# Kernel tuning notes

Hardware: AMD Instinct MI355X
Metric: run time of the kernel (lower is better)

The kernel has to match this reference:

```python
import jax, jax.numpy as jnp
import numpy as np


def setup_inputs() -> dict:
    key = jax.random.key(0)
    kx, ka, kb, kc = jax.random.split(key, 4)
    B, S = 32, 16384
    K, L, M = 4, 10, 10
    return {
        "x": jax.random.normal(kx, (B, S, 2), dtype=jnp.float32),
        "a": jax.random.normal(ka, (K, L), dtype=jnp.float32),
        "b": jax.random.normal(kb, (K, L, M), dtype=jnp.float32),
        "c": jax.random.normal(kc, (K, L, M), dtype=jnp.float32),  # unused in forward (matches original)
    }


def reference(x, a, b, c):
    # Generalized Memory Polynomial.
    # y[n] = sum_{k,l} a[k,l] * x[n-L+1+l] * |x[n-L+1+l]|^k
    #      + sum_{k,l,m} b[k,l,m] * x[n-l] * |x[n-l-(m+1)]|^(k+1), for n >= L+M, else 0.
    K, L = a.shape
    M = b.shape[2]
    B, S, _ = x.shape
    D = L + M  # max shift needed is (L-1)+M < D

    xc = x[..., 0] + 1j * x[..., 1]  # (B, S) complex64

    # Shifted views: xs[d][:, n] = x[:, n-d] (zero for n < d; masked out below anyway).
    xp = jnp.pad(xc, ((0, 0), (D - 1, 0)))
    xs = jnp.stack([xp[:, D - 1 - d: D - 1 - d + S] for d in range(D)])  # (D, B, S)

    absx = jnp.abs(xs)  # (D, B, S)
    # pows[k, d] = |x[n-d]|^k, k in 0..K
    pows = absx[None] ** jnp.arange(K + 1, dtype=x.dtype)[:, None, None, None]  # (K+1, D, B, S)

    # Term 1: shift d = L-1-l  ->  coefficient a[k, L-1-d]
    a_rev = a[:, ::-1]  # (K, L), a_rev[k, d] = a[k, L-1-d]
    coef1 = jnp.einsum('kd,kdbs->dbs', a_rev, pows[:K, :L])  # real (L, B, S)
    y = jnp.einsum('dbs,dbs->bs', coef1.astype(xc.dtype), xs[:L])  # complex (B, S)

    # Term 2: y += sum_{k,l,m} b[k,l,m] * x[n-l] * |x[n-l-m-1]|^(k+1)
    for l in range(L):  # small structural loop (L=10)
        coef2 = jnp.einsum('km,kmbs->bs', b[:, l, :], pows[1:, l + 1: l + 1 + M])  # real (B, S)
        y = y + coef2.astype(xc.dtype) * xs[l]

    # Only n >= L+M is written in the original (y initialized to zero elsewhere).
    mask = (jnp.arange(S) >= D).astype(x.dtype)  # (S,)
    y = y * mask

    out = jnp.stack([jnp.real(y), jnp.imag(y)], axis=-1)  # (B, S, 2)
    return out
```

## Files before the change

kernel.cpp:

```cpp
#include <hip/hip_runtime.h>


typedef short short8 __attribute__((ext_vector_type(8)));
typedef float f32x4 __attribute__((ext_vector_type(4)));

constexpr int S_FIXED = 16384;
constexpr int BLK = 256;
constexpr int TILE = 512;

__device__ __forceinline__ unsigned short bfc(float f) {
    union { float f; unsigned u; } v; v.f = f;
    const unsigned u = v.u;
    return (unsigned short)((u + 0x7FFFu + ((u >> 16) & 1u)) >> 16);
}

__device__ __forceinline__ short8 mk8(ushort4 lo, ushort4 hi) {
    union { ushort4 u[2]; short8 s; } x;
    x.u[0] = lo; x.u[1] = hi;
    return x.s;
}

__global__ __launch_bounds__(BLK) void gmp_mfma(
    const float* __restrict__ x,
    const float* __restrict__ a,
    const float* __restrict__ b,
    float* __restrict__ out,
    int S)
{
    __shared__ alignas(16) unsigned short th[16][64];
    __shared__ alignas(16) ushort4 qr[4][160];
    __shared__ alignas(16) float wl[4][10][148];

    const int t = threadIdx.x;
    const int wid = t >> 6, lane = t & 63;
    const int m = lane & 15, h = lane >> 4;
    const int blocksPerRow = S / TILE;
    const int brow = blockIdx.x / blocksPerRow;
    const int s0   = (blockIdx.x % blocksPerRow) * TILE;
    const int s0w  = s0 + 128 * wid;
    const int vb   = s0w - 12;

    for (int idx = t; idx < 1024; idx += BLK) {
        const int col = idx >> 6, f = idx & 63;
        float v = 0.f;
        if (col < 10 && f < 44) {
            const int j = f >> 2, c = f & 3;
            if (j == 0) { if (c < 3) v = a[(c + 1) * 10 + (9 - col)]; }
            else v = b[c * 100 + col * 10 + (j - 1)];
        }
        th[col][f] = bfc(v);
    }

    const float2* __restrict__ xr2 =
        reinterpret_cast<const float2*>(x) + (size_t)brow * S;
    for (int i = lane; i < 160; i += 64) {
        const int p = vb + 143 - i;
        float xre = 0.f, xim = 0.f;
        if (p >= 0 && p < S) { const float2 v = xr2[p]; xre = v.x; xim = v.y; }
        const float m2 = xre * xre + xim * xim;
        const float r  = __builtin_amdgcn_sqrtf(m2);
        ushort4 q;
        q.x = bfc(r); q.y = bfc(m2); q.z = bfc(m2 * r); q.w = bfc(m2 * m2);
        qr[wid][i] = q;
    }
    __syncthreads();

    const short8 bfr0 = *reinterpret_cast<const short8*>(&th[m][8 * h]);
    const short8 bfr1 = *reinterpret_cast<const short8*>(&th[m][8 * h + 32]);

    #pragma unroll
    for (int g = 0; g < 9; ++g) {
        const int i1 = 143 - 16 * g - m + 2 * h;
        const short8 af0 = mk8(qr[wid][i1],     qr[wid][i1 + 1]);
        const short8 af1 = mk8(qr[wid][i1 + 8], qr[wid][i1 + 9]);
        f32x4 acc = {0.f, 0.f, 0.f, 0.f};
        acc = __builtin_amdgcn_mfma_f32_16x16x32_bf16(af0, bfr0, acc, 0, 0, 0);
        acc = __builtin_amdgcn_mfma_f32_16x16x32_bf16(af1, bfr1, acc, 0, 0, 0);
        if (m < 10)
            *reinterpret_cast<f32x4*>(&wl[wid][m][16 * g + 4 * h]) = acc;
    }

    const int sa0 = s0w + 2 * lane;
    const float4* __restrict__ xr4 =
        reinterpret_cast<const float4*>(x) + (size_t)brow * (S / 2);
    float xf[24];
    {
        const int base4 = (sa0 - 10) / 2;
        #pragma unroll
        for (int n = 0; n < 6; ++n) {
            int idx = base4 + n;
            if (idx < 0) idx = 0;
            const float4 f4 = xr4[idx];
            xf[4 * n + 0] = f4.x; xf[4 * n + 1] = f4.y;
            xf[4 * n + 2] = f4.z; xf[4 * n + 3] = f4.w;
        }
    }
    float yr0 = 0.f, yi0 = 0.f, yr1 = 0.f, yi1 = 0.f;
    #pragma unroll
    for (int l = 0; l < 10; ++l) {
        const float bl = a[9 - l];
        const float w0 = wl[wid][l][2 * lane + 12 - l] + bl;
        const float w1 = wl[wid][l][2 * lane + 13 - l] + bl;
        const int wp = 10 - l;
        yr0 += w0 * xf[2 * wp];     yi0 += w0 * xf[2 * wp + 1];
        yr1 += w1 * xf[2 * wp + 2]; yi1 += w1 * xf[2 * wp + 3];
    }
    const bool k0 = sa0 >= 20, k1 = (sa0 + 1) >= 20;
    const float4 o = make_float4(k0 ? yr0 : 0.f, k0 ? yi0 : 0.f,
                                 k1 ? yr1 : 0.f, k1 ? yi1 : 0.f);
    reinterpret_cast<float4*>(out)[((size_t)brow * S + sa0) / 2] = o;
}

extern "C" void kernel_launch(void* const* d_in, const int* in_sizes, int n_in,
                              void* d_out, int out_size, void* d_ws, size_t ws_size,
                              hipStream_t stream) {
    const float* x = (const float*)d_in[0];
    const float* a = (const float*)d_in[1];
    const float* b = (const float*)d_in[2];
    float* out = (float*)d_out;

    const int S = S_FIXED;
    const int B = in_sizes[0] / (2 * S);
    const int nblocks = B * (S / TILE);

    gmp_mfma<<<dim3(nblocks), dim3(BLK), 0, stream>>>(x, a, b, out, S);
}
```

Before: 13.38 us.

## Halve tile size so each lane computes one output sample

Shrinks the per-block tile from 512 to 256 samples, so each wave covers 64 samples and each lane produces one complex output instead of two. The shared buffers and MFMA group count shrink to match, and the epilogue loads ten float2 values per lane instead of six float4 values. This doubles the block count for more parallelism and less serial work per thread. In exchange the 12-sample halo and the coefficient setup are repeated more often relative to useful work, and global loads and stores become narrower.

```diff
diff --git a/kernel.cpp b/kernel.cpp
--- a/kernel.cpp
+++ b/kernel.cpp
@@ -6,7 +6,11 @@
 
 constexpr int S_FIXED = 16384;
 constexpr int BLK = 256;
-constexpr int TILE = 512;
+constexpr int TILE = 256;
+constexpr int GROUPS = 5;
+constexpr int IMAX = 79;
+constexpr int QRN = 96;
+constexpr int WLW = 84;
 
 __device__ __forceinline__ unsigned short bfc(float f) {
     union { float f; unsigned u; } v; v.f = f;
@@ -28,8 +32,8 @@
     int S)
 {
     __shared__ alignas(16) unsigned short th[16][64];
-    __shared__ alignas(16) ushort4 qr[4][160];
-    __shared__ alignas(16) float wl[4][10][148];
+    __shared__ alignas(16) ushort4 qr[4][QRN];
+    __shared__ alignas(16) float wl[4][10][WLW];
 
     const int t = threadIdx.x;
     const int wid = t >> 6, lane = t & 63;
@@ -37,7 +41,7 @@
     const int blocksPerRow = S / TILE;
     const int brow = blockIdx.x / blocksPerRow;
     const int s0   = (blockIdx.x % blocksPerRow) * TILE;
-    const int s0w  = s0 + 128 * wid;
+    const int s0w  = s0 + 64 * wid;
     const int vb   = s0w - 12;
 
     for (int idx = t; idx < 1024; idx += BLK) {
@@ -53,8 +57,8 @@
 
     const float2* __restrict__ xr2 =
         reinterpret_cast<const float2*>(x) + (size_t)brow * S;
-    for (int i = lane; i < 160; i += 64) {
-        const int p = vb + 143 - i;
+    for (int i = lane; i < QRN; i += 64) {
+        const int p = vb + IMAX - i;
         float xre = 0.f, xim = 0.f;
         if (p >= 0 && p < S) { const float2 v = xr2[p]; xre = v.x; xim = v.y; }
         const float m2 = xre * xre + xim * xim;
@@ -69,8 +73,8 @@
     const short8 bfr1 = *reinterpret_cast<const short8*>(&th[m][8 * h + 32]);
 
     #pragma unroll
-    for (int g = 0; g < 9; ++g) {
-        const int i1 = 143 - 16 * g - m + 2 * h;
+    for (int g = 0; g < GROUPS; ++g) {
+        const int i1 = IMAX - 16 * g - m + 2 * h;
         const short8 af0 = mk8(qr[wid][i1],     qr[wid][i1 + 1]);
         const short8 af1 = mk8(qr[wid][i1 + 8], qr[wid][i1 + 9]);
         f32x4 acc = {0.f, 0.f, 0.f, 0.f};
@@ -80,35 +84,25 @@
             *reinterpret_cast<f32x4*>(&wl[wid][m][16 * g + 4 * h]) = acc;
     }
 
-    const int sa0 = s0w + 2 * lane;
-    const float4* __restrict__ xr4 =
-        reinterpret_cast<const float4*>(x) + (size_t)brow * (S / 2);
-    float xf[24];
-    {
-        const int base4 = (sa0 - 10) / 2;
-        #pragma unroll
-        for (int n = 0; n < 6; ++n) {
-            int idx = base4 + n;
-            if (idx < 0) idx = 0;
-            const float4 f4 = xr4[idx];
-            xf[4 * n + 0] = f4.x; xf[4 * n + 1] = f4.y;
-            xf[4 * n + 2] = f4.z; xf[4 * n + 3] = f4.w;
-        }
+    const int sa0 = s0w + lane;
+    float xre[10], xim[10];
+    #pragma unroll
+    for (int i = 0; i < 10; ++i) {
+        int p = sa0 - 9 + i;
+        if (p < 0) p = 0;
+        const float2 v = xr2[p];
+        xre[i] = v.x; xim[i] = v.y;
     }
-    float yr0 = 0.f, yi0 = 0.f, yr1 = 0.f, yi1 = 0.f;
+    float yr = 0.f, yi = 0.f;
     #pragma unroll
     for (int l = 0; l < 10; ++l) {
-        const float bl = a[9 - l];
-        const float w0 = wl[wid][l][2 * lane + 12 - l] + bl;
-        const float w1 = wl[wid][l][2 * lane + 13 - l] + bl;
-        const int wp = 10 - l;
-        yr0 += w0 * xf[2 * wp];     yi0 += w0 * xf[2 * wp + 1];
-        yr1 += w1 * xf[2 * wp + 2]; yi1 += w1 * xf[2 * wp + 3];
+        const float w = wl[wid][l][lane + 12 - l] + a[9 - l];
+        yr += w * xre[9 - l];
+        yi += w * xim[9 - l];
     }
-    const bool k0 = sa0 >= 20, k1 = (sa0 + 1) >= 20;
-    const float4 o = make_float4(k0 ? yr0 : 0.f, k0 ? yi0 : 0.f,
-                                 k1 ? yr1 : 0.f, k1 ? yi1 : 0.f);
-    reinterpret_cast<float4*>(out)[((size_t)brow * S + sa0) / 2] = o;
+    const bool keep = sa0 >= 20;
+    const float2 o = make_float2(keep ? yr : 0.f, keep ? yi : 0.f);
+    reinterpret_cast<float2*>(out)[(size_t)brow * S + sa0] = o;
 }
 
 extern "C" void kernel_launch(void* const* d_in, const int* in_sizes, int n_in,
```

Result: faster. 12.29 us (-8.1%).
